# Kernel optimization log

Measured on AMD Instinct MI355X. Metric: run time of the kernel, lower is better.

## Reference

```python
import jax, jax.numpy as jnp
import numpy as np

NUM_HEADS = 8
WINDOW = 128  # num_previous_frames
EPS = 1e-5


def setup_inputs() -> dict:
    key = jax.random.key(0)
    ks = jax.random.split(key, 5)
    B, T, E = 8, 1024, 512
    x = jax.random.normal(ks[0], (B, T, E), dtype=jnp.float32)
    x_lengths = jax.random.randint(ks[1], (B,), 1, T + 1).astype(jnp.int32)
    gamma = jnp.ones((E,), dtype=jnp.float32)
    beta = jnp.zeros((E,), dtype=jnp.float32)
    sc_in = 1.0 / np.sqrt(E)
    w_in = jax.random.normal(ks[2], (3 * E, E), dtype=jnp.float32) * sc_in
    b_in = jnp.zeros((3 * E,), dtype=jnp.float32)
    w_out = jax.random.normal(ks[3], (E, E), dtype=jnp.float32) * sc_in
    b_out = jnp.zeros((E,), dtype=jnp.float32)
    return {"x": x, "x_lengths": x_lengths, "gamma": gamma, "beta": beta,
            "w_in": w_in, "b_in": b_in, "w_out": w_out, "b_out": b_out}


def _forward(x, gamma, beta, w_in, b_in, w_out, b_out):
    B, T, E = x.shape
    H = NUM_HEADS
    D = E // H
    # Timewise LayerNorm: normalize over channel dim per (batch, time)
    mu = jnp.mean(x, axis=-1, keepdims=True)
    var = jnp.mean(jnp.square(x - mu), axis=-1, keepdims=True)
    xn = (x - mu) * jax.lax.rsqrt(var + EPS) * gamma + beta
    # in-projection: qkv packed
    qkv = xn @ w_in.T + b_in  # [B,T,3E]
    q, k, v = jnp.split(qkv, 3, axis=-1)
    q = q.reshape(B, T, H, D)
    k = k.reshape(B, T, H, D)
    v = v.reshape(B, T, H, D)
    scale = 1.0 / np.sqrt(D)
    scores = jnp.einsum('bqhd,bkhd->bhqk', q * scale, k)  # [B,H,T,T]
    # banded causal mask: allow j in [i-WINDOW, i]
    i = jnp.arange(T)[:, None]
    j = jnp.arange(T)[None, :]
    allowed = (j <= i) & (j >= i - WINDOW)
    scores = jnp.where(allowed[None, None], scores, -jnp.inf)
    attn = jax.nn.softmax(scores, axis=-1)
    ctx = jnp.einsum('bhqk,bkhd->bqhd', attn, v).reshape(B, T, E)
    out = ctx @ w_out.T + b_out
    return out  # dropout is identity in eval mode


def reference(x, x_lengths, gamma, beta, w_in, b_in, w_out, b_out):
    del x_lengths  # unused by the original forward (no key_padding_mask passed)
    return _forward(x, gamma, beta, w_in, b_in, w_out, b_out)
```

## Files before the change

### kernel.cpp

```cpp
#include <hip/hip_runtime.h>
#include <stdint.h>

typedef __bf16 bf16;
typedef __bf16 bf16x8 __attribute__((ext_vector_type(8)));
typedef float f32x4 __attribute__((ext_vector_type(4)));

#define MFMA_16x16x32(a, b, c) __builtin_amdgcn_mfma_f32_16x16x32_bf16((a), (b), (c), 0, 0, 0)

__device__ __forceinline__ void gl_lds16(const bf16* g, bf16* l) {
    __builtin_amdgcn_global_load_lds(
        (const __attribute__((address_space(1))) void*)g,
        (__attribute__((address_space(3))) void*)l, 16, 0, 0);
}

__global__ __launch_bounds__(256) void prep_kernel(const float* __restrict__ x,
                                                   const float* __restrict__ gamma,
                                                   const float* __restrict__ beta,
                                                   const float* __restrict__ w_in,
                                                   const float* __restrict__ w_out,
                                                   bf16* __restrict__ xn,
                                                   bf16* __restrict__ cw_in,
                                                   bf16* __restrict__ cw_out) {
    const int bid = blockIdx.x;
    if (bid < 2048) {
        const int lane = threadIdx.x & 63;
        const int row = (bid << 2) + (threadIdx.x >> 6);
        const size_t base = (size_t)row * 512 + lane * 8;
        const float* xf = x + base;
        float4 a = *(const float4*)xf;
        float4 b = *(const float4*)(xf + 4);
        float f[8] = {a.x, a.y, a.z, a.w, b.x, b.y, b.z, b.w};
        float s = 0.f;
#pragma unroll
        for (int j = 0; j < 8; ++j) s += f[j];
#pragma unroll
        for (int off = 32; off >= 1; off >>= 1) s += __shfl_xor(s, off, 64);
        const float mu = s * (1.0f / 512.0f);
        float vs = 0.f;
#pragma unroll
        for (int j = 0; j < 8; ++j) { float d = f[j] - mu; vs += d * d; }
#pragma unroll
        for (int off = 32; off >= 1; off >>= 1) vs += __shfl_xor(vs, off, 64);
        const float rstd = rsqrtf(vs * (1.0f / 512.0f) + 1e-5f);
        float4 g0 = *(const float4*)(gamma + lane * 8);
        float4 g1 = *(const float4*)(gamma + lane * 8 + 4);
        float4 b0 = *(const float4*)(beta + lane * 8);
        float4 b1 = *(const float4*)(beta + lane * 8 + 4);
        float gg[8] = {g0.x, g0.y, g0.z, g0.w, g1.x, g1.y, g1.z, g1.w};
        float bb[8] = {b0.x, b0.y, b0.z, b0.w, b1.x, b1.y, b1.z, b1.w};
        bf16x8 o;
#pragma unroll
        for (int j = 0; j < 8; ++j)
            o[j] = (bf16)((f[j] - mu) * rstd * gg[j] + bb[j]);
        *(bf16x8*)(xn + base) = o;
    } else {
        const float* src;
        bf16* dst;
        int base;
        if (bid < 2432) { src = w_in;  dst = cw_in;  base = (bid - 2048) * 2048; }
        else            { src = w_out; dst = cw_out; base = (bid - 2432) * 2048; }
        const int i = base + threadIdx.x * 8;
        float4 a = *(const float4*)(src + i);
        float4 b = *(const float4*)(src + i + 4);
        float f[8] = {a.x, a.y, a.z, a.w, b.x, b.y, b.z, b.w};
        bf16x8 o;
#pragma unroll
        for (int j = 0; j < 8; ++j) o[j] = (bf16)f[j];
        *(bf16x8*)(dst + i) = o;
    }
}

template <int TM, typename OT>
__global__ __launch_bounds__(256) void gemm_bt(const bf16* __restrict__ A,
                                               const bf16* __restrict__ B,
                                               const float* __restrict__ bias,
                                               OT* __restrict__ C,
                                               int N, int K) {
    constexpr int MI = TM / 32;
    constexpr int NCA = TM * 8;
    __shared__ alignas(16) bf16 As[TM * 64];
    __shared__ alignas(16) bf16 Bs[128 * 64];
    const int tid = threadIdx.x;
    const int lane = tid & 63;
    const int wid = tid >> 6;
    const int wm = (wid >> 1) * (TM / 2), wn = (wid & 1) * 64;
    const int m0 = blockIdx.y * TM, n0 = blockIdx.x * 128;
    const int l15 = lane & 15, l16 = lane >> 4;

    f32x4 acc[MI][4] = {};

    const bf16* Abase = A + (size_t)m0 * K;
    const bf16* Bbase = B + (size_t)n0 * K;

    for (int k0 = 0; k0 < K; k0 += 64) {
#pragma unroll
        for (int c = tid; c < NCA; c += 256) {
            const int p = c / (TM * 4);
            const int r = (c % (TM * 4)) >> 2;
            const int ko = (c & 3) * 8 + p * 32;
            gl_lds16(Abase + (size_t)r * K + k0 + ko, &As[c * 8]);
        }
#pragma unroll
        for (int c = tid; c < 1024; c += 256) {
            const int p = c >> 9;
            const int r = (c & 511) >> 2;
            const int ko = (c & 3) * 8 + p * 32;
            gl_lds16(Bbase + (size_t)r * K + k0 + ko, &Bs[c * 8]);
        }
        __syncthreads();
#pragma unroll
        for (int h = 0; h < 2; ++h) {
            bf16x8 af[MI], bfr[4];
#pragma unroll
            for (int t = 0; t < MI; ++t)
                af[t] = *(const bf16x8*)&As[h * (TM * 32) + (wm + t * 16 + l15) * 32 + l16 * 8];
#pragma unroll
            for (int t = 0; t < 4; ++t)
                bfr[t] = *(const bf16x8*)&Bs[h * 4096 + (wn + t * 16 + l15) * 32 + l16 * 8];
#pragma unroll
            for (int i = 0; i < MI; ++i)
#pragma unroll
                for (int j = 0; j < 4; ++j)
                    acc[i][j] = MFMA_16x16x32(af[i], bfr[j], acc[i][j]);
        }
        __syncthreads();
    }

#pragma unroll
    for (int j = 0; j < 4; ++j) {
        const int col = n0 + wn + j * 16 + l15;
        const float bv = bias[col];
#pragma unroll
        for (int i = 0; i < MI; ++i) {
            const int rbase = m0 + wm + i * 16 + l16 * 4;
#pragma unroll
            for (int r = 0; r < 4; ++r)
                C[(size_t)(rbase + r) * N + col] = (OT)(acc[i][j][r] + bv);
        }
    }
}

#define KS_STRIDE 72
#define VN_STRIDE 74
#define PW_STRIDE 40

__global__ __launch_bounds__(256) void attn_kernel(const bf16* __restrict__ qkv,
                                                   bf16* __restrict__ ctx) {
    __shared__ alignas(16) bf16 Ks[192 * KS_STRIDE];
    __shared__ alignas(16) bf16 Vn[192 * VN_STRIDE];
    __shared__ alignas(16) bf16 Pbuf[4 * 16 * PW_STRIDE];

    const int tid = threadIdx.x;
    const int lane = tid & 63, wid = tid >> 6;
    const int l15 = lane & 15, l16 = lane >> 4;
    const int bh = blockIdx.y, b = bh >> 3, h = bh & 7;
    const int q0 = blockIdx.x * 64;
    const int kv0 = (q0 > 128) ? (q0 - 128) : 0;
    const int nk = q0 + 64 - kv0;
    const size_t tokbase = (size_t)b * 1024;

    for (int c = tid; c < nk * 8; c += 256) {
        const int kk = c >> 3, dc = (c & 7) * 8;
        const bf16* src = qkv + (tokbase + kv0 + kk) * 1536 + h * 64 + dc;
        uint4 kw = *(const uint4*)(src + 512);
        *(uint4*)&Ks[kk * KS_STRIDE + dc] = kw;
        uint4 vw = *(const uint4*)(src + 1024);
        uint* vdst = (uint*)&Vn[kk * VN_STRIDE + dc];
        vdst[0] = vw.x; vdst[1] = vw.y; vdst[2] = vw.z; vdst[3] = vw.w;
    }

    const int qt0 = q0 + wid * 16;
    const bf16* qptr = qkv + (tokbase + qt0 + l15) * 1536 + h * 64;
    bf16x8 qa0 = *(const bf16x8*)(qptr + l16 * 8);
    bf16x8 qa1 = *(const bf16x8*)(qptr + 32 + l16 * 8);

    __syncthreads();

    bf16* Pw = &Pbuf[wid * 16 * PW_STRIDE];
    f32x4 of[4] = {};
    float mst[4], lst[4];
#pragma unroll
    for (int r = 0; r < 4; ++r) { mst[r] = -1e30f; lst[r] = 0.f; }

    const int ktstart = ((qt0 > 128) ? (qt0 - 128) : 0) & ~31;
    for (int kt = ktstart; kt <= qt0 + 15; kt += 32) {
        const int krel = kt - kv0;
        f32x4 s0 = {}, s1 = {};
        {
            const bf16* kb0 = &Ks[(krel + l15) * KS_STRIDE + l16 * 8];
            const bf16* kb1 = kb0 + 16 * KS_STRIDE;
            s0 = MFMA_16x16x32(qa0, *(const bf16x8*)kb0, s0);
            s0 = MFMA_16x16x32(qa1, *(const bf16x8*)(kb0 + 32), s0);
            s1 = MFMA_16x16x32(qa0, *(const bf16x8*)kb1, s1);
            s1 = MFMA_16x16x32(qa1, *(const bf16x8*)(kb1 + 32), s1);
        }
        float e0[4], e1[4];
#pragma unroll
        for (int r = 0; r < 4; ++r) {
            const int qa = qt0 + l16 * 4 + r;
            const int kg0 = kt + l15;
            const int kg1 = kg0 + 16;
            const bool ok0 = (kg0 <= qa) && (kg0 >= qa - 128);
            const bool ok1 = (kg1 <= qa) && (kg1 >= qa - 128);
            float v0 = ok0 ? s0[r] * 0.125f : -1e30f;
            float v1 = ok1 ? s1[r] * 0.125f : -1e30f;
            float mx = fmaxf(v0, v1);
#pragma unroll
            for (int off = 1; off < 16; off <<= 1)
                mx = fmaxf(mx, __shfl_xor(mx, off, 64));
            const float mnew = fmaxf(mst[r], mx);
            const float alpha = __expf(mst[r] - mnew);
            e0[r] = ok0 ? __expf(v0 - mnew) : 0.f;
            e1[r] = ok1 ? __expf(v1 - mnew) : 0.f;
            float rs = e0[r] + e1[r];
#pragma unroll
            for (int off = 1; off < 16; off <<= 1)
                rs += __shfl_xor(rs, off, 64);
            lst[r] = lst[r] * alpha + rs;
            mst[r] = mnew;
#pragma unroll
            for (int nt = 0; nt < 4; ++nt) of[nt][r] *= alpha;
        }
#pragma unroll
        for (int r = 0; r < 4; ++r) {
            const int q = l16 * 4 + r;
            Pw[q * PW_STRIDE + l15] = (bf16)e0[r];
            Pw[q * PW_STRIDE + 16 + l15] = (bf16)e1[r];
        }
        __asm__ volatile("s_waitcnt lgkmcnt(0)" ::: "memory");
        bf16x8 pa = *(const bf16x8*)&Pw[l15 * PW_STRIDE + l16 * 8];
        int row[8];
#pragma unroll
        for (int j = 0; j < 8; ++j) {
            int rr = krel + l16 * 8 + j;
            row[j] = (rr < nk) ? rr : (nk - 1);
        }
#pragma unroll
        for (int nt = 0; nt < 4; ++nt) {
            bf16x8 vb;
#pragma unroll
            for (int j = 0; j < 8; ++j)
                vb[j] = Vn[row[j] * VN_STRIDE + nt * 16 + l15];
            of[nt] = MFMA_16x16x32(pa, vb, of[nt]);
        }
        __asm__ volatile("s_waitcnt lgkmcnt(0)" ::: "memory");
    }

    float linv[4];
#pragma unroll
    for (int r = 0; r < 4; ++r) linv[r] = 1.0f / lst[r];
    bf16* cbase = ctx + (tokbase + qt0) * 512 + h * 64;
#pragma unroll
    for (int nt = 0; nt < 4; ++nt)
#pragma unroll
        for (int r = 0; r < 4; ++r) {
            const int q = l16 * 4 + r;
            cbase[(size_t)q * 512 + nt * 16 + l15] = (bf16)(of[nt][r] * linv[r]);
        }
}

extern "C" void kernel_launch(void* const* d_in, const int* in_sizes, int n_in,
                              void* d_out, int out_size, void* d_ws, size_t ws_size,
                              hipStream_t stream) {
    const float* x     = (const float*)d_in[0];
    const float* gamma = (const float*)d_in[2];
    const float* beta  = (const float*)d_in[3];
    const float* w_in  = (const float*)d_in[4];
    const float* b_in  = (const float*)d_in[5];
    const float* w_out = (const float*)d_in[6];
    const float* b_out = (const float*)d_in[7];
    float* out = (float*)d_out;

    char* ws = (char*)d_ws;
    bf16* cw_in  = (bf16*)ws;
    bf16* cw_out = cw_in + 786432;
    bf16* xn     = (bf16*)(ws + (4u << 20));
    bf16* qkv    = (bf16*)(ws + (12u << 20));
    bf16* ctx    = xn;

    prep_kernel<<<2560, 256, 0, stream>>>(x, gamma, beta, w_in, w_out, xn, cw_in, cw_out);
    gemm_bt<128, bf16><<<dim3(12, 64), 256, 0, stream>>>(xn, cw_in, b_in, qkv, 1536, 512);
    attn_kernel<<<dim3(16, 64), 256, 0, stream>>>(qkv, ctx);
    gemm_bt<64, float><<<dim3(4, 128), 256, 0, stream>>>(ctx, cw_out, b_out, out, 512, 512);
}
```

Before: 139.1 us.

## Widen attention key tile to 64 with band skipping and vectorize GEMM epilogue

The GEMM swaps the MFMA operands so each lane holds four consecutive output columns, which allows float4 bias loads and 4-wide vector stores in the epilogue. The attention loop now steps 64 keys at a time instead of 32, skips 16-key groups that fall entirely outside the banded causal window, and skips the PV MFMA half when it is all masked. It also raises wave priority around the MFMA sections. This halves the number of softmax reduction rounds and cuts scalar global stores, at the cost of more registers and extra branching.

```diff
diff --git a/kernel.cpp b/kernel.cpp
--- a/kernel.cpp
+++ b/kernel.cpp
@@ -2,6 +2,7 @@
 #include <stdint.h>
 
 typedef __bf16 bf16;
+typedef __bf16 bf16x4 __attribute__((ext_vector_type(4)));
 typedef __bf16 bf16x8 __attribute__((ext_vector_type(8)));
 typedef float f32x4 __attribute__((ext_vector_type(4)));
 
@@ -121,28 +122,40 @@
             for (int i = 0; i < MI; ++i)
 #pragma unroll
                 for (int j = 0; j < 4; ++j)
-                    acc[i][j] = MFMA_16x16x32(af[i], bfr[j], acc[i][j]);
+                    acc[i][j] = MFMA_16x16x32(bfr[j], af[i], acc[i][j]);
         }
         __syncthreads();
     }
 
 #pragma unroll
     for (int j = 0; j < 4; ++j) {
-        const int col = n0 + wn + j * 16 + l15;
-        const float bv = bias[col];
+        const int colb = n0 + wn + j * 16 + (l16 << 2);
+        const float4 bv = *(const float4*)(bias + colb);
 #pragma unroll
         for (int i = 0; i < MI; ++i) {
-            const int rbase = m0 + wm + i * 16 + l16 * 4;
-#pragma unroll
-            for (int r = 0; r < 4; ++r)
-                C[(size_t)(rbase + r) * N + col] = (OT)(acc[i][j][r] + bv);
+            const int row = m0 + wm + i * 16 + l15;
+            if constexpr (sizeof(OT) == 2) {
+                bf16x4 o;
+                o[0] = (bf16)(acc[i][j][0] + bv.x);
+                o[1] = (bf16)(acc[i][j][1] + bv.y);
+                o[2] = (bf16)(acc[i][j][2] + bv.z);
+                o[3] = (bf16)(acc[i][j][3] + bv.w);
+                *(bf16x4*)&C[(size_t)row * N + colb] = o;
+            } else {
+                float4 o;
+                o.x = acc[i][j][0] + bv.x;
+                o.y = acc[i][j][1] + bv.y;
+                o.z = acc[i][j][2] + bv.z;
+                o.w = acc[i][j][3] + bv.w;
+                *(float4*)&C[(size_t)row * N + colb] = o;
+            }
         }
     }
 }
 
 #define KS_STRIDE 72
 #define VN_STRIDE 74
-#define PW_STRIDE 40
+#define PW_STRIDE 72
 
 __global__ __launch_bounds__(256) void attn_kernel(const bf16* __restrict__ qkv,
                                                    bf16* __restrict__ ctx) {
@@ -182,37 +195,47 @@
 #pragma unroll
     for (int r = 0; r < 4; ++r) { mst[r] = -1e30f; lst[r] = 0.f; }
 
-    const int ktstart = ((qt0 > 128) ? (qt0 - 128) : 0) & ~31;
-    for (int kt = ktstart; kt <= qt0 + 15; kt += 32) {
+    const int ktstart = ((qt0 > 128) ? (qt0 - 128) : 0) & ~63;
+    for (int kt = ktstart; kt <= qt0 + 15; kt += 64) {
         const int krel = kt - kv0;
-        f32x4 s0 = {}, s1 = {};
-        {
-            const bf16* kb0 = &Ks[(krel + l15) * KS_STRIDE + l16 * 8];
-            const bf16* kb1 = kb0 + 16 * KS_STRIDE;
-            s0 = MFMA_16x16x32(qa0, *(const bf16x8*)kb0, s0);
-            s0 = MFMA_16x16x32(qa1, *(const bf16x8*)(kb0 + 32), s0);
-            s1 = MFMA_16x16x32(qa0, *(const bf16x8*)kb1, s1);
-            s1 = MFMA_16x16x32(qa1, *(const bf16x8*)(kb1 + 32), s1);
-        }
-        float e0[4], e1[4];
+        int kgn = ((qt0 + 15 - kt) >> 4) + 1;
+        if (kgn > 4) kgn = 4;
+        const int dlo = qt0 - 128 - kt;
+        const int kglo = (dlo > 0) ? (dlo >> 4) : 0;
+
+        f32x4 s[4] = {};
+        __builtin_amdgcn_s_setprio(1);
+#pragma unroll
+        for (int kg = 0; kg < 4; ++kg) {
+            if (kg >= kglo && kg < kgn) {
+                const bf16* kb = &Ks[(krel + kg * 16 + l15) * KS_STRIDE + l16 * 8];
+                s[kg] = MFMA_16x16x32(qa0, *(const bf16x8*)kb, s[kg]);
+                s[kg] = MFMA_16x16x32(qa1, *(const bf16x8*)(kb + 32), s[kg]);
+            }
+        }
+        __builtin_amdgcn_s_setprio(0);
+
 #pragma unroll
         for (int r = 0; r < 4; ++r) {
             const int qa = qt0 + l16 * 4 + r;
-            const int kg0 = kt + l15;
-            const int kg1 = kg0 + 16;
-            const bool ok0 = (kg0 <= qa) && (kg0 >= qa - 128);
-            const bool ok1 = (kg1 <= qa) && (kg1 >= qa - 128);
-            float v0 = ok0 ? s0[r] * 0.125f : -1e30f;
-            float v1 = ok1 ? s1[r] * 0.125f : -1e30f;
-            float mx = fmaxf(v0, v1);
+            float v[4];
+#pragma unroll
+            for (int kg = 0; kg < 4; ++kg) {
+                const int key = kt + kg * 16 + l15;
+                const bool ok = (key <= qa) && (key >= qa - 128);
+                v[kg] = ok ? s[kg][r] * 0.125f : -1e30f;
+            }
+            float mx = fmaxf(fmaxf(v[0], v[1]), fmaxf(v[2], v[3]));
 #pragma unroll
             for (int off = 1; off < 16; off <<= 1)
                 mx = fmaxf(mx, __shfl_xor(mx, off, 64));
             const float mnew = fmaxf(mst[r], mx);
             const float alpha = __expf(mst[r] - mnew);
-            e0[r] = ok0 ? __expf(v0 - mnew) : 0.f;
-            e1[r] = ok1 ? __expf(v1 - mnew) : 0.f;
-            float rs = e0[r] + e1[r];
+            const float e0 = __expf(v[0] - mnew);
+            const float e1 = __expf(v[1] - mnew);
+            const float e2 = __expf(v[2] - mnew);
+            const float e3 = __expf(v[3] - mnew);
+            float rs = (e0 + e1) + (e2 + e3);
 #pragma unroll
             for (int off = 1; off < 16; off <<= 1)
                 rs += __shfl_xor(rs, off, 64);
@@ -220,29 +243,52 @@
             mst[r] = mnew;
 #pragma unroll
             for (int nt = 0; nt < 4; ++nt) of[nt][r] *= alpha;
-        }
-#pragma unroll
-        for (int r = 0; r < 4; ++r) {
             const int q = l16 * 4 + r;
-            Pw[q * PW_STRIDE + l15] = (bf16)e0[r];
-            Pw[q * PW_STRIDE + 16 + l15] = (bf16)e1[r];
+            Pw[q * PW_STRIDE + l15] = (bf16)e0;
+            Pw[q * PW_STRIDE + 16 + l15] = (bf16)e1;
+            Pw[q * PW_STRIDE + 32 + l15] = (bf16)e2;
+            Pw[q * PW_STRIDE + 48 + l15] = (bf16)e3;
         }
         __asm__ volatile("s_waitcnt lgkmcnt(0)" ::: "memory");
-        bf16x8 pa = *(const bf16x8*)&Pw[l15 * PW_STRIDE + l16 * 8];
-        int row[8];
-#pragma unroll
-        for (int j = 0; j < 8; ++j) {
-            int rr = krel + l16 * 8 + j;
-            row[j] = (rr < nk) ? rr : (nk - 1);
-        }
-#pragma unroll
-        for (int nt = 0; nt < 4; ++nt) {
-            bf16x8 vb;
-#pragma unroll
-            for (int j = 0; j < 8; ++j)
-                vb[j] = Vn[row[j] * VN_STRIDE + nt * 16 + l15];
-            of[nt] = MFMA_16x16x32(pa, vb, of[nt]);
-        }
+
+        const bool haveA = (kglo < 2);
+        const bool haveB = (kgn > 2);
+        __builtin_amdgcn_s_setprio(1);
+        if (haveA) {
+            bf16x8 pa = *(const bf16x8*)&Pw[l15 * PW_STRIDE + l16 * 8];
+            int row[8];
+#pragma unroll
+            for (int j = 0; j < 8; ++j) {
+                int rr = krel + l16 * 8 + j;
+                row[j] = (rr < nk) ? rr : (nk - 1);
+            }
+#pragma unroll
+            for (int nt = 0; nt < 4; ++nt) {
+                bf16x8 vb;
+#pragma unroll
+                for (int j = 0; j < 8; ++j)
+                    vb[j] = Vn[row[j] * VN_STRIDE + nt * 16 + l15];
+                of[nt] = MFMA_16x16x32(pa, vb, of[nt]);
+            }
+        }
+        if (haveB) {
+            bf16x8 pa = *(const bf16x8*)&Pw[l15 * PW_STRIDE + 32 + l16 * 8];
+            int row[8];
+#pragma unroll
+            for (int j = 0; j < 8; ++j) {
+                int rr = krel + 32 + l16 * 8 + j;
+                row[j] = (rr < nk) ? rr : (nk - 1);
+            }
+#pragma unroll
+            for (int nt = 0; nt < 4; ++nt) {
+                bf16x8 vb;
+#pragma unroll
+                for (int j = 0; j < 8; ++j)
+                    vb[j] = Vn[row[j] * VN_STRIDE + nt * 16 + l15];
+                of[nt] = MFMA_16x16x32(pa, vb, of[nt]);
+            }
+        }
+        __builtin_amdgcn_s_setprio(0);
         __asm__ volatile("s_waitcnt lgkmcnt(0)" ::: "memory");
     }
 
```

Measured after the change: 145.7 us. 4.8% more time.
